# Kernel optimization log

Measured on AMD Instinct MI355X. Metric: run time of the kernel, lower is better.

## Reference

```python
import jax, jax.numpy as jnp
import numpy as np

SEQ, BATCH, IN, H = 1024, 32, 1024, 1024


def setup_inputs() -> dict:
    key = jax.random.key(0)
    ks = jax.random.split(key, 7)
    s_in = 1.0 / np.sqrt(IN)
    s_h = 1.0 / np.sqrt(H)
    return {
        "X": jax.random.normal(ks[0], (SEQ, BATCH, IN), jnp.float32),
        "W_iozfux": jax.random.normal(ks[1], (IN, 5 * H), jnp.float32) * s_in,
        "b_iozfux": jax.random.normal(ks[2], (5 * H,), jnp.float32) * s_in,
        "W_iozfh": jax.random.normal(ks[3], (H, 4 * H), jnp.float32) * s_h,
        "b_iozfh": jax.random.normal(ks[4], (4 * H,), jnp.float32) * s_h,
        "W_um": jax.random.normal(ks[5], (H, H), jnp.float32) * s_h,
        "b_um": jax.random.normal(ks[6], (H,), jnp.float32) * s_h,
    }


def reference(X, W_iozfux, b_iozfux, W_iozfh, b_iozfh, W_um, b_um):
    seq_len, batch, _ = X.shape
    hdim = W_iozfh.shape[0]
    # Input projection has no recurrence: do one big matmul over all timesteps.
    iozfux = jnp.einsum('sbi,ig->sbg', X, W_iozfux) + b_iozfux  # (S, B, 5H)

    h0 = jnp.zeros((batch, hdim), X.dtype)
    c0 = jnp.zeros((batch, hdim), X.dtype)
    ct0 = jnp.tanh(c0)

    def step(carry, ux):
        h, c, c_tanh = carry
        iozf = jax.nn.sigmoid(ux[:, :4 * hdim] + h @ W_iozfh + b_iozfh)
        i, o, z, f = jnp.split(iozf, 4, axis=1)
        u = jnp.tanh(ux[:, 4 * hdim:] + (z * c_tanh) @ W_um + b_um)
        c_new = i * u + f * c
        ct_new = jnp.tanh(c_new)
        h_new = o * ct_new
        return (h_new, c_new, ct_new), h_new

    (h_n, c_n, _), output = jax.lax.scan(step, (h0, c0, ct0), iozfux)
    return output, (h_n[None], c_n[None])
```

## Files before the change

kernel.cpp:

```cpp
#include <hip/hip_runtime.h>


typedef unsigned short u16;
typedef __attribute__((ext_vector_type(4))) float f32x4;
typedef __attribute__((ext_vector_type(8))) short s16x8;
typedef __attribute__((ext_vector_type(8))) unsigned short u16x8;

#define SEQ   1024
#define BATCH 32
#define HDIM  1024
#define GBLK  64

__device__ __forceinline__ u16 f2bf(float f) {
    unsigned u = __builtin_bit_cast(unsigned, f);
    return (u16)((u + 0x7FFFu + ((u >> 16) & 1u)) >> 16);
}
__device__ __forceinline__ float bf2f(u16 h) {
    return __builtin_bit_cast(float, (unsigned)h << 16);
}

__device__ __forceinline__ u16x8 gload_cc(const u16* p) {
    u16x8 v;
    asm volatile("global_load_dwordx4 %0, %1, off sc0 sc1" : "=&v"(v) : "v"(p));
    return v;
}
__device__ __forceinline__ void vmwait0() {
    asm volatile("s_waitcnt vmcnt(0)" ::: "memory");
    __builtin_amdgcn_sched_barrier(0);
}
__device__ __forceinline__ void gstore_cc(u16* p, u16 d) {
    unsigned x = d;
    asm volatile("global_store_short %0, %1, off sc0 sc1" :: "v"(p), "v"(x) : "memory");
}

__global__ void prep_w0(const float* __restrict__ W, const float* __restrict__ b_ux,
                        const float* __restrict__ b_h, const float* __restrict__ b_um,
                        u16* __restrict__ W0p, float* __restrict__ biasp) {
    int p = blockIdx.x;
    int g = p / 80, r = p % 80, gate = r >> 4, j = r & 15;
    int n = 16 * g + j;
    int c = (gate < 4) ? gate * 1024 + n : 4096 + n;
    for (int k = threadIdx.x; k < 1024; k += 256)
        W0p[(long)p * 1024 + k] = f2bf(W[(long)k * 5120 + c]);
    if (threadIdx.x == 0)
        biasp[p] = b_ux[c] + ((gate < 4) ? b_h[gate * 1024 + n] : b_um[n]);
}

__global__ void prep_w1(const float* __restrict__ W, u16* __restrict__ W1p) {
    int qq = blockIdx.x;
    int g = qq >> 6, r = qq & 63, gate = r >> 4, j = r & 15;
    int n = 16 * g + j;
    int c = gate * 1024 + n;
    for (int k = threadIdx.x; k < 1024; k += 256)
        W1p[(long)qq * 1024 + k] = f2bf(W[(long)k * 4096 + c]);
}

__global__ void prep_w2(const float* __restrict__ W, u16* __restrict__ W2p) {
    int n = blockIdx.x;
    for (int k = threadIdx.x; k < 1024; k += 256)
        W2p[(long)n * 1024 + k] = f2bf(W[(long)k * 1024 + n]);
}

__global__ void __launch_bounds__(256) gemm_in(const float* __restrict__ X,
                                               const u16* __restrict__ W0p,
                                               const float* __restrict__ biasp,
                                               u16* __restrict__ Yp) {
    __shared__ u16 As[128 * 40];
    __shared__ u16 Bs[64 * 40];
    const int tid = threadIdx.x, lane = tid & 63, w = tid >> 6;
    const int m = lane & 15, q = lane >> 4;
    const int m0 = blockIdx.y * 128, n0 = blockIdx.x * 64;

    f32x4 acc[2][4];
#pragma unroll
    for (int a = 0; a < 2; ++a)
#pragma unroll
        for (int b = 0; b < 4; ++b) acc[a][b] = (f32x4){0.f, 0.f, 0.f, 0.f};

    const int ar = tid >> 1, as = (tid & 1) * 16;
    const int br = tid >> 2, bs = (tid & 3) * 8;

    for (int k0 = 0; k0 < 1024; k0 += 32) {
        const float* xp = X + (long)(m0 + ar) * 1024 + k0 + as;
        float4 x0 = *(const float4*)(xp);
        float4 x1 = *(const float4*)(xp + 4);
        float4 x2 = *(const float4*)(xp + 8);
        float4 x3 = *(const float4*)(xp + 12);
        u16x8 pa, pb;
        pa[0]=f2bf(x0.x); pa[1]=f2bf(x0.y); pa[2]=f2bf(x0.z); pa[3]=f2bf(x0.w);
        pa[4]=f2bf(x1.x); pa[5]=f2bf(x1.y); pa[6]=f2bf(x1.z); pa[7]=f2bf(x1.w);
        pb[0]=f2bf(x2.x); pb[1]=f2bf(x2.y); pb[2]=f2bf(x2.z); pb[3]=f2bf(x2.w);
        pb[4]=f2bf(x3.x); pb[5]=f2bf(x3.y); pb[6]=f2bf(x3.z); pb[7]=f2bf(x3.w);
        u16x8 bv = *(const u16x8*)(W0p + (long)(n0 + br) * 1024 + k0 + bs);

        *(u16x8*)&As[ar * 40 + as]     = pa;
        *(u16x8*)&As[ar * 40 + as + 8] = pb;
        *(u16x8*)&Bs[br * 40 + bs]     = bv;
        __syncthreads();

        s16x8 a0 = *(const s16x8*)&As[(w * 32 + m) * 40 + q * 8];
        s16x8 a1 = *(const s16x8*)&As[(w * 32 + 16 + m) * 40 + q * 8];
#pragma unroll
        for (int nt = 0; nt < 4; ++nt) {
            s16x8 b = *(const s16x8*)&Bs[(nt * 16 + m) * 40 + q * 8];
            acc[0][nt] = __builtin_amdgcn_mfma_f32_16x16x32_bf16(a0, b, acc[0][nt], 0, 0, 0);
            acc[1][nt] = __builtin_amdgcn_mfma_f32_16x16x32_bf16(a1, b, acc[1][nt], 0, 0, 0);
        }
        __syncthreads();
    }
#pragma unroll
    for (int mt = 0; mt < 2; ++mt)
#pragma unroll
        for (int nt = 0; nt < 4; ++nt) {
            int p = n0 + nt * 16 + m;
            int gg = p / 80, rr = p - gg * 80;
            float bias = biasp[p];
#pragma unroll
            for (int r = 0; r < 4; ++r) {
                int row = m0 + w * 32 + mt * 16 + q * 4 + r;
                int s = row >> 5, b = row & 31;
                Yp[(((long)gg * 1024 + s) * 32 + b) * 80 + rr] = f2bf(acc[mt][nt][r] + bias);
            }
        }
}

__device__ __forceinline__ void gridbar(unsigned* flags, unsigned phase, int g) {
    asm volatile("s_waitcnt vmcnt(0)" ::: "memory");
    __syncthreads();
    if (threadIdx.x < 64) {
        if (threadIdx.x == 0)
            __hip_atomic_store(&flags[g * 32], phase, __ATOMIC_RELEASE,
                               __HIP_MEMORY_SCOPE_AGENT);
        for (;;) {
            unsigned v = __hip_atomic_load(&flags[threadIdx.x * 32], __ATOMIC_RELAXED,
                                           __HIP_MEMORY_SCOPE_AGENT);
            if (__ballot(v >= phase) == ~0ull) break;
            __builtin_amdgcn_s_sleep(1);
        }
    }
    __syncthreads();
}

__global__ void __launch_bounds__(256, 1) ulstm_rec(const u16* __restrict__ W1p,
                                                    const u16* __restrict__ W2p,
                                                    const u16* __restrict__ Yp,
                                                    u16* h_buf, u16* v_buf,
                                                    float* __restrict__ out,
                                                    unsigned* flags) {
    __shared__ u16 stage[32 * 1032];
    __shared__ u16 ys[2][2560];
    __shared__ float gl[4][32][17];
    __shared__ float c_l[32][17], ct_l[32][17];

    const int g = blockIdx.x, tid = threadIdx.x, lane = tid & 63, w = tid >> 6;
    const int m = lane & 15, q = lane >> 4;

    for (int i = tid; i < 512; i += 256) {
        int row = i >> 4, col = i & 15;
        c_l[row][col] = 0.f; ct_l[row][col] = 0.f;
        gstore_cc(&h_buf[row * 1024 + g * 16 + col], (u16)0);
    }
    {
        const u16x8* src = (const u16x8*)(Yp + (long)g * 1024 * 2560);
        for (int i = tid; i < 320; i += 256)
            *(u16x8*)&ys[0][i * 8] = __builtin_nontemporal_load(&src[i]);
    }
    unsigned phase = 1;
    gridbar(flags, phase, g);

    for (int t = 0; t < SEQ; ++t) {
        const u16* ysb = ys[t & 1];

        u16x8 hreg[16];
#pragma unroll
        for (int j = 0; j < 16; ++j) {
            int cch = tid + j * 256;
            int r = cch >> 7, kc = cch & 127;
            hreg[j] = gload_cc(&h_buf[r * 1024 + kc * 8]);
        }
        if (t + 1 < SEQ) {
            const u16x8* src = (const u16x8*)(Yp + ((long)g * 1024 + t + 1) * 2560);
            u16* dst = ys[(t + 1) & 1];
            for (int i = tid; i < 320; i += 256)
                *(u16x8*)&dst[i * 8] = __builtin_nontemporal_load(&src[i]);
        }
        vmwait0();
#pragma unroll
        for (int j = 0; j < 16; ++j) {
            int cch = tid + j * 256;
            int r = cch >> 7, kc = cch & 127;
            *(u16x8*)&stage[r * 1032 + kc * 8] = hreg[j];
        }
        __syncthreads();

        f32x4 acc0 = (f32x4){0.f,0.f,0.f,0.f}, acc1 = (f32x4){0.f,0.f,0.f,0.f};
        {
            const int brow = g * 64 + w * 16 + m;
            const u16* wp = W1p + (long)brow * 1024;
#pragma unroll 8
            for (int kc = 0; kc < 32; ++kc) {
                int k0 = kc * 32 + q * 8;
                s16x8 a0 = *(const s16x8*)&stage[m * 1032 + k0];
                s16x8 a1 = *(const s16x8*)&stage[(16 + m) * 1032 + k0];
                s16x8 b  = *(const s16x8*)&wp[k0];
                acc0 = __builtin_amdgcn_mfma_f32_16x16x32_bf16(a0, b, acc0, 0, 0, 0);
                acc1 = __builtin_amdgcn_mfma_f32_16x16x32_bf16(a1, b, acc1, 0, 0, 0);
            }
        }
#pragma unroll
        for (int r = 0; r < 4; ++r) {
            int row0 = q * 4 + r, row1 = row0 + 16;
            float p0 = acc0[r] + bf2f(ysb[row0 * 80 + w * 16 + m]);
            float p1 = acc1[r] + bf2f(ysb[row1 * 80 + w * 16 + m]);
            float g0 = 1.f / (1.f + __expf(-p0));
            float g1 = 1.f / (1.f + __expf(-p1));
            gl[w][row0][m] = g0;
            gl[w][row1][m] = g1;
            if (w == 2) {
                gstore_cc(&v_buf[row0 * 1024 + g * 16 + m], f2bf(g0 * ct_l[row0][m]));
                gstore_cc(&v_buf[row1 * 1024 + g * 16 + m], f2bf(g1 * ct_l[row1][m]));
            }
        }
        gridbar(flags, ++phase, g);

        u16x8 vreg[16];
#pragma unroll
        for (int j = 0; j < 16; ++j) {
            int cch = tid + j * 256;
            int r = cch >> 7, kc = cch & 127;
            vreg[j] = gload_cc(&v_buf[r * 1024 + kc * 8]);
        }
        vmwait0();
#pragma unroll
        for (int j = 0; j < 16; ++j) {
            int cch = tid + j * 256;
            int r = cch >> 7, kc = cch & 127;
            *(u16x8*)&stage[r * 1032 + kc * 8] = vreg[j];
        }
        __syncthreads();

        if (w < 2) {
            f32x4 acc = (f32x4){0.f,0.f,0.f,0.f};
            const u16* wp = W2p + (long)(g * 16 + m) * 1024;
#pragma unroll 8
            for (int kc = 0; kc < 32; ++kc) {
                int k0 = kc * 32 + q * 8;
                s16x8 a = *(const s16x8*)&stage[(w * 16 + m) * 1032 + k0];
                s16x8 b = *(const s16x8*)&wp[k0];
                acc = __builtin_amdgcn_mfma_f32_16x16x32_bf16(a, b, acc, 0, 0, 0);
            }
#pragma unroll
            for (int r = 0; r < 4; ++r) {
                int row = w * 16 + q * 4 + r;
                float up = acc[r] + bf2f(ysb[row * 80 + 64 + m]);
                float eu = __expf(2.f * up);
                float u = 1.f - 2.f / (eu + 1.f);
                float iv = gl[0][row][m], ov = gl[1][row][m], fv = gl[3][row][m];
                float cv = c_l[row][m];
                float cn = iv * u + fv * cv;
                float ec = __expf(2.f * cn);
                float ctn = 1.f - 2.f / (ec + 1.f);
                float hn = ov * ctn;
                c_l[row][m] = cn;
                ct_l[row][m] = ctn;
                gstore_cc(&h_buf[row * 1024 + g * 16 + m], f2bf(hn));
                __builtin_nontemporal_store(hn, &out[(long)(t * 32 + row) * 1024 + g * 16 + m]);
                if (t == SEQ - 1) {
                    out[33554432l + row * 1024 + g * 16 + m] = hn;
                    out[33554432l + 32768 + row * 1024 + g * 16 + m] = cn;
                }
            }
        }
        gridbar(flags, ++phase, g);
    }
}

extern "C" void kernel_launch(void* const* d_in, const int* in_sizes, int n_in,
                              void* d_out, int out_size, void* d_ws, size_t ws_size,
                              hipStream_t stream) {
    (void)in_sizes; (void)n_in; (void)out_size; (void)ws_size;
    const float* X  = (const float*)d_in[0];
    const float* W0 = (const float*)d_in[1];
    const float* b0 = (const float*)d_in[2];
    const float* W1 = (const float*)d_in[3];
    const float* b1 = (const float*)d_in[4];
    const float* W2 = (const float*)d_in[5];
    const float* b2 = (const float*)d_in[6];
    float* out = (float*)d_out;
    char* ws = (char*)d_ws;

    u16*   Yp    = (u16*)(ws);
    u16*   W0p   = (u16*)(ws + 335544320l);
    u16*   W1p   = (u16*)(ws + 346030080l);
    u16*   W2p   = (u16*)(ws + 354418688l);
    float* biasp = (float*)(ws + 356515840l);
    u16*   h_buf = (u16*)(ws + 356536320l);
    u16*   v_buf = (u16*)(ws + 356601856l);
    unsigned* flags = (unsigned*)(ws + 356667392l);

    hipMemsetAsync(flags, 0, 8192, stream);
    prep_w0<<<5120, 256, 0, stream>>>(W0, b0, b1, b2, W0p, biasp);
    prep_w1<<<4096, 256, 0, stream>>>(W1, W1p);
    prep_w2<<<1024, 256, 0, stream>>>(W2, W2p);
    gemm_in<<<dim3(80, 256), 256, 0, stream>>>(X, W0p, biasp, Yp);

    void* args[] = { (void*)&W1p, (void*)&W2p, (void*)&Yp,
                     (void*)&h_buf, (void*)&v_buf, (void*)&out, (void*)&flags };
    hipLaunchCooperativeKernel(reinterpret_cast<void*>(ulstm_rec),
                               dim3(GBLK), dim3(256), args, 0, stream);
}
```

Before: 14.72 ms.

## Replace grid barriers with flag-tagged data exchange and split-phase barriers

Drops the two full grid barriers per timestep. Each block now publishes its h and v slices as 16-byte packets of seven bf16 values plus a step tag. Consumers poll those packets directly until every tag matches, so the data itself serves as the synchronization signal. Two relaxed counter arrays act as split-phase barriers against buffer reuse, and their waits are overlapped with the gate matmuls. This removes barrier round-trip latency per step, but relies on relaxed ordering and sixteen-bit step tags being correct. It also reuses part of the W0p workspace region for the exchange buffers.

```diff
diff --git a/kernel.cpp b/kernel.cpp
--- a/kernel.cpp
+++ b/kernel.cpp
@@ -19,18 +19,12 @@
     return __builtin_bit_cast(float, (unsigned)h << 16);
 }
 
-__device__ __forceinline__ u16x8 gload_cc(const u16* p) {
-    u16x8 v;
-    asm volatile("global_load_dwordx4 %0, %1, off sc0 sc1" : "=&v"(v) : "v"(p));
-    return v;
-}
 __device__ __forceinline__ void vmwait0() {
     asm volatile("s_waitcnt vmcnt(0)" ::: "memory");
     __builtin_amdgcn_sched_barrier(0);
 }
-__device__ __forceinline__ void gstore_cc(u16* p, u16 d) {
-    unsigned x = d;
-    asm volatile("global_store_short %0, %1, off sc0 sc1" :: "v"(p), "v"(x) : "memory");
+__device__ __forceinline__ void gstore_cc16(u16* p, u16x8 d) {
+    asm volatile("global_store_dwordx4 %0, %1, off sc0 sc1" :: "v"(p), "v"(d) : "memory");
 }
 
 __global__ void prep_w0(const float* __restrict__ W, const float* __restrict__ b_ux,
@@ -124,33 +118,51 @@
         }
 }
 
-__device__ __forceinline__ void gridbar(unsigned* flags, unsigned phase, int g) {
-    asm volatile("s_waitcnt vmcnt(0)" ::: "memory");
-    __syncthreads();
-    if (threadIdx.x < 64) {
-        if (threadIdx.x == 0)
-            __hip_atomic_store(&flags[g * 32], phase, __ATOMIC_RELEASE,
-                               __HIP_MEMORY_SCOPE_AGENT);
-        for (;;) {
-            unsigned v = __hip_atomic_load(&flags[threadIdx.x * 32], __ATOMIC_RELAXED,
-                                           __HIP_MEMORY_SCOPE_AGENT);
-            if (__ballot(v >= phase) == ~0ull) break;
-            __builtin_amdgcn_s_sleep(1);
-        }
-    }
-    __syncthreads();
+#define ISSUE1(i, ofs)                                                        \
+    if (!((valid >> i) & 1))                                                  \
+        asm volatile("global_load_dwordx4 %0, %1, off offset:" ofs " sc0 sc1" \
+                     : "=&v"(ch[i]) : "v"(lanebase));
+
+__device__ __forceinline__ void poll_unpack(const u16* lanebase, unsigned valid,
+                                            u16 want, u16* stage_, int tid) {
+    u16x8 ch[24];
+    int rounds = 0;
+    while (valid != 0xFFFFFFu) {
+        if (rounds++) __builtin_amdgcn_s_sleep(1);
+        ISSUE1(0, "0")   ISSUE1(1, "16")   ISSUE1(2, "32")   ISSUE1(3, "48")
+        ISSUE1(4, "64")  ISSUE1(5, "80")   ISSUE1(6, "96")   ISSUE1(7, "112")
+        ISSUE1(8, "128") ISSUE1(9, "144")  ISSUE1(10, "160") ISSUE1(11, "176")
+        ISSUE1(12, "192") ISSUE1(13, "208") ISSUE1(14, "224") ISSUE1(15, "240")
+        ISSUE1(16, "256") ISSUE1(17, "272") ISSUE1(18, "288") ISSUE1(19, "304")
+        ISSUE1(20, "320") ISSUE1(21, "336") ISSUE1(22, "352") ISSUE1(23, "368")
+        vmwait0();
+#pragma unroll
+        for (int i = 0; i < 24; ++i) {
+            if (!((valid >> i) & 1) && ch[i][7] == want) {
+                valid |= 1u << i;
+                const int grp = tid * 8 + i / 3;
+                const int row = grp >> 6, gg = grp & 63;
+                const int col0 = gg * 16 + (i % 3) * 7;
+                const int n = (i % 3 == 2) ? 2 : 7;
+#pragma unroll
+                for (int j = 0; j < 7; ++j)
+                    if (j < n) stage_[row * 1032 + col0 + j] = ch[i][j];
+            }
+        }
+    }
 }
 
 __global__ void __launch_bounds__(256, 1) ulstm_rec(const u16* __restrict__ W1p,
                                                     const u16* __restrict__ W2p,
                                                     const u16* __restrict__ Yp,
-                                                    u16* h_buf, u16* v_buf,
+                                                    u16* hx, u16* vx,
                                                     float* __restrict__ out,
-                                                    unsigned* flags) {
+                                                    unsigned* bar1, unsigned* bar2) {
     __shared__ u16 stage[32 * 1032];
     __shared__ u16 ys[2][2560];
     __shared__ float gl[4][32][17];
     __shared__ float c_l[32][17], ct_l[32][17];
+    __shared__ u16 h_l[32 * 17 + 8];
 
     const int g = blockIdx.x, tid = threadIdx.x, lane = tid & 63, w = tid >> 6;
     const int m = lane & 15, q = lane >> 4;
@@ -158,40 +170,53 @@
     for (int i = tid; i < 512; i += 256) {
         int row = i >> 4, col = i & 15;
         c_l[row][col] = 0.f; ct_l[row][col] = 0.f;
-        gstore_cc(&h_buf[row * 1024 + g * 16 + col], (u16)0);
+    }
+    for (int i = tid; i < 32 * 17 + 8; i += 256) h_l[i] = 0;
+
+    if (tid < 96) {
+        int row = (tid * 171) >> 9, c = tid - 3 * row;
+        u16x8 z = (u16x8){0, 0, 0, 0, 0, 0, 0, 0};
+        z[7] = (u16)1;
+        gstore_cc16(hx + (row * 64 + g) * 24 + c * 8, z);
     }
     {
         const u16x8* src = (const u16x8*)(Yp + (long)g * 1024 * 2560);
         for (int i = tid; i < 320; i += 256)
             *(u16x8*)&ys[0][i * 8] = __builtin_nontemporal_load(&src[i]);
     }
-    unsigned phase = 1;
-    gridbar(flags, phase, g);
+
+    unsigned selfmask = 0;
+#pragma unroll
+    for (int i = 0; i < 24; ++i)
+        if (((tid * 8 + i / 3) & 63) == g) selfmask |= 1u << i;
+    const int prow = tid >> 3, pcp = (tid & 7) * 2;
+
+    __syncthreads();
 
     for (int t = 0; t < SEQ; ++t) {
         const u16* ysb = ys[t & 1];
-
-        u16x8 hreg[16];
-#pragma unroll
-        for (int j = 0; j < 16; ++j) {
-            int cch = tid + j * 256;
-            int r = cch >> 7, kc = cch & 127;
-            hreg[j] = gload_cc(&h_buf[r * 1024 + kc * 8]);
-        }
+        const u16 want = (u16)(t + 1);
+
         if (t + 1 < SEQ) {
             const u16x8* src = (const u16x8*)(Yp + ((long)g * 1024 + t + 1) * 2560);
             u16* dst = ys[(t + 1) & 1];
             for (int i = tid; i < 320; i += 256)
                 *(u16x8*)&dst[i * 8] = __builtin_nontemporal_load(&src[i]);
         }
-        vmwait0();
-#pragma unroll
-        for (int j = 0; j < 16; ++j) {
-            int cch = tid + j * 256;
-            int r = cch >> 7, kc = cch & 127;
-            *(u16x8*)&stage[r * 1032 + kc * 8] = hreg[j];
-        }
-        __syncthreads();
+
+        stage[prow * 1032 + g * 16 + pcp]     = h_l[prow * 17 + pcp];
+        stage[prow * 1032 + g * 16 + pcp + 1] = h_l[prow * 17 + pcp + 1];
+        poll_unpack(hx + (t & 1) * 49152 + tid * 192, selfmask, want, stage, tid);
+        __syncthreads();
+
+        unsigned fl = 0;
+        if (w == 0) {
+            if (tid == 0)
+                __hip_atomic_store(&bar1[g * 32], (unsigned)(t + 1),
+                                   __ATOMIC_RELAXED, __HIP_MEMORY_SCOPE_AGENT);
+            fl = __hip_atomic_load(&bar2[lane * 32], __ATOMIC_RELAXED,
+                                   __HIP_MEMORY_SCOPE_AGENT);
+        }
 
         f32x4 acc0 = (f32x4){0.f,0.f,0.f,0.f}, acc1 = (f32x4){0.f,0.f,0.f,0.f};
         {
@@ -214,30 +239,44 @@
             float p1 = acc1[r] + bf2f(ysb[row1 * 80 + w * 16 + m]);
             float g0 = 1.f / (1.f + __expf(-p0));
             float g1 = 1.f / (1.f + __expf(-p1));
-            gl[w][row0][m] = g0;
-            gl[w][row1][m] = g1;
             if (w == 2) {
-                gstore_cc(&v_buf[row0 * 1024 + g * 16 + m], f2bf(g0 * ct_l[row0][m]));
-                gstore_cc(&v_buf[row1 * 1024 + g * 16 + m], f2bf(g1 * ct_l[row1][m]));
-            }
-        }
-        gridbar(flags, ++phase, g);
-
-        u16x8 vreg[16];
-#pragma unroll
-        for (int j = 0; j < 16; ++j) {
-            int cch = tid + j * 256;
-            int r = cch >> 7, kc = cch & 127;
-            vreg[j] = gload_cc(&v_buf[r * 1024 + kc * 8]);
-        }
-        vmwait0();
-#pragma unroll
-        for (int j = 0; j < 16; ++j) {
-            int cch = tid + j * 256;
-            int r = cch >> 7, kc = cch & 127;
-            *(u16x8*)&stage[r * 1032 + kc * 8] = vreg[j];
-        }
-        __syncthreads();
+                gl[2][row0][m] = g0 * ct_l[row0][m];
+                gl[2][row1][m] = g1 * ct_l[row1][m];
+            } else {
+                gl[w][row0][m] = g0;
+                gl[w][row1][m] = g1;
+            }
+        }
+        if (w == 0 && t >= 1) {
+            while (__ballot((int)fl >= t - 1) != ~0ull) {
+                __builtin_amdgcn_s_sleep(1);
+                fl = __hip_atomic_load(&bar2[lane * 32], __ATOMIC_RELAXED,
+                                       __HIP_MEMORY_SCOPE_AGENT);
+            }
+        }
+        __syncthreads();
+
+        if (tid < 96) {
+            int row = (tid * 171) >> 9, c = tid - 3 * row;
+            u16x8 pk;
+#pragma unroll
+            for (int j = 0; j < 7; ++j) pk[j] = f2bf(gl[2][row][c * 7 + j]);
+            pk[7] = want;
+            gstore_cc16(vx + (t & 1) * 49152 + (row * 64 + g) * 24 + c * 8, pk);
+        }
+
+        stage[prow * 1032 + g * 16 + pcp]     = f2bf(gl[2][prow][pcp]);
+        stage[prow * 1032 + g * 16 + pcp + 1] = f2bf(gl[2][prow][pcp + 1]);
+        poll_unpack(vx + (t & 1) * 49152 + tid * 192, selfmask, want, stage, tid);
+        __syncthreads();
+
+        if (tid == 0)
+            __hip_atomic_store(&bar2[g * 32], (unsigned)(t + 1),
+                               __ATOMIC_RELAXED, __HIP_MEMORY_SCOPE_AGENT);
+        unsigned fl2 = 0;
+        if (w == 3)
+            fl2 = __hip_atomic_load(&bar1[lane * 32], __ATOMIC_RELAXED,
+                                    __HIP_MEMORY_SCOPE_AGENT);
 
         if (w < 2) {
             f32x4 acc = (f32x4){0.f,0.f,0.f,0.f};
@@ -263,7 +302,7 @@
                 float hn = ov * ctn;
                 c_l[row][m] = cn;
                 ct_l[row][m] = ctn;
-                gstore_cc(&h_buf[row * 1024 + g * 16 + m], f2bf(hn));
+                h_l[row * 17 + m] = f2bf(hn);
                 __builtin_nontemporal_store(hn, &out[(long)(t * 32 + row) * 1024 + g * 16 + m]);
                 if (t == SEQ - 1) {
                     out[33554432l + row * 1024 + g * 16 + m] = hn;
@@ -271,7 +310,23 @@
                 }
             }
         }
-        gridbar(flags, ++phase, g);
+        if (w == 3) {
+            while (__ballot((int)fl2 >= t) != ~0ull) {
+                __builtin_amdgcn_s_sleep(1);
+                fl2 = __hip_atomic_load(&bar1[lane * 32], __ATOMIC_RELAXED,
+                                        __HIP_MEMORY_SCOPE_AGENT);
+            }
+        }
+        __syncthreads();
+
+        if (t + 1 < SEQ && tid < 96) {
+            int row = (tid * 171) >> 9, c = tid - 3 * row;
+            u16x8 pk;
+#pragma unroll
+            for (int j = 0; j < 7; ++j) pk[j] = h_l[row * 17 + c * 7 + j];
+            pk[7] = (u16)(t + 2);
+            gstore_cc16(hx + ((t + 1) & 1) * 49152 + (row * 64 + g) * 24 + c * 8, pk);
+        }
     }
 }
 
@@ -294,18 +349,21 @@
     u16*   W1p   = (u16*)(ws + 346030080l);
     u16*   W2p   = (u16*)(ws + 354418688l);
     float* biasp = (float*)(ws + 356515840l);
-    u16*   h_buf = (u16*)(ws + 356536320l);
-    u16*   v_buf = (u16*)(ws + 356601856l);
-    unsigned* flags = (unsigned*)(ws + 356667392l);
-
-    hipMemsetAsync(flags, 0, 8192, stream);
+
+    u16*   hx    = (u16*)(ws + 335544320l);
+    u16*   vx    = (u16*)(ws + 335740928l);
+    unsigned* bar1 = (unsigned*)(ws + 335937536l);
+    unsigned* bar2 = (unsigned*)(ws + 335945728l);
+
     prep_w0<<<5120, 256, 0, stream>>>(W0, b0, b1, b2, W0p, biasp);
     prep_w1<<<4096, 256, 0, stream>>>(W1, W1p);
     prep_w2<<<1024, 256, 0, stream>>>(W2, W2p);
     gemm_in<<<dim3(80, 256), 256, 0, stream>>>(X, W0p, biasp, Yp);
+    hipMemsetAsync(hx, 0, 409600, stream);
 
     void* args[] = { (void*)&W1p, (void*)&W2p, (void*)&Yp,
-                     (void*)&h_buf, (void*)&v_buf, (void*)&out, (void*)&flags };
+                     (void*)&hx, (void*)&vx, (void*)&out,
+                     (void*)&bar1, (void*)&bar2 };
     hipLaunchCooperativeKernel(reinterpret_cast<void*>(ulstm_rec),
                                dim3(GBLK), dim3(256), args, 0, stream);
 }
```

Measured after the change: 23.01 ms. 1.56x slower.

## Consolidate recurrent LSTM into 16 workgroups of 1024 threads

Applied to the files above, without the earlier changes.

The persistent recurrent kernel now runs on 16 cooperative blocks of 1024 threads instead of 64 blocks of 256. Each block owns 64 hidden columns, so one fewer tier of blocks takes part in each grid barrier. Each block also stages h/v once per step for four times the work, which cuts redundant global reads of the shared state. The Y prefetch is held in registers and written to LDS after the barrier, and the barrier polls only active flags. The trade-off is fewer CUs doing the per-step matmul and larger per-block LDS and register pressure.

```diff
diff --git a/kernel.cpp b/kernel.cpp
--- a/kernel.cpp
+++ b/kernel.cpp
@@ -9,7 +9,7 @@
 #define SEQ   1024
 #define BATCH 32
 #define HDIM  1024
-#define GBLK  64
+#define GBLK  16
 
 __device__ __forceinline__ u16 f2bf(float f) {
     unsigned u = __builtin_bit_cast(unsigned, f);
@@ -128,12 +128,15 @@
     asm volatile("s_waitcnt vmcnt(0)" ::: "memory");
     __syncthreads();
     if (threadIdx.x < 64) {
+        unsigned v;
         if (threadIdx.x == 0)
             __hip_atomic_store(&flags[g * 32], phase, __ATOMIC_RELEASE,
                                __HIP_MEMORY_SCOPE_AGENT);
         for (;;) {
-            unsigned v = __hip_atomic_load(&flags[threadIdx.x * 32], __ATOMIC_RELAXED,
-                                           __HIP_MEMORY_SCOPE_AGENT);
+            v = (threadIdx.x < GBLK)
+                    ? __hip_atomic_load(&flags[threadIdx.x * 32], __ATOMIC_RELAXED,
+                                        __HIP_MEMORY_SCOPE_AGENT)
+                    : phase;
             if (__ballot(v >= phase) == ~0ull) break;
             __builtin_amdgcn_s_sleep(1);
         }
@@ -141,133 +144,159 @@
     __syncthreads();
 }
 
-__global__ void __launch_bounds__(256, 1) ulstm_rec(const u16* __restrict__ W1p,
-                                                    const u16* __restrict__ W2p,
-                                                    const u16* __restrict__ Yp,
-                                                    u16* h_buf, u16* v_buf,
-                                                    float* __restrict__ out,
-                                                    unsigned* flags) {
-    __shared__ u16 stage[32 * 1032];
-    __shared__ u16 ys[2][2560];
-    __shared__ float gl[4][32][17];
-    __shared__ float c_l[32][17], ct_l[32][17];
+__global__ void __launch_bounds__(1024, 1) ulstm_rec(const u16* __restrict__ W1p,
+                                                     const u16* __restrict__ W2p,
+                                                     const u16* __restrict__ Yp,
+                                                     u16* h_buf, u16* v_buf,
+                                                     float* __restrict__ out,
+                                                     unsigned* flags) {
+    __shared__ u16 stage[32 * 1028];
+    __shared__ u16 ys[2][4][2560];
+    __shared__ float gl[4][32][66];
+    __shared__ float c_l[32][66], ct_l[32][66];
 
     const int g = blockIdx.x, tid = threadIdx.x, lane = tid & 63, w = tid >> 6;
     const int m = lane & 15, q = lane >> 4;
-
-    for (int i = tid; i < 512; i += 256) {
-        int row = i >> 4, col = i & 15;
-        c_l[row][col] = 0.f; ct_l[row][col] = 0.f;
-        gstore_cc(&h_buf[row * 1024 + g * 16 + col], (u16)0);
+    const int nb = g * 64;
+
+    for (int i = tid; i < 32 * 66; i += 1024) {
+        ((float*)c_l)[i] = 0.f; ((float*)ct_l)[i] = 0.f;
+    }
+    for (int i = tid; i < 2048; i += 1024) {
+        int row = i >> 6, col = i & 63;
+        gstore_cc(&h_buf[row * 1024 + nb + col], (u16)0);
     }
     {
-        const u16x8* src = (const u16x8*)(Yp + (long)g * 1024 * 2560);
-        for (int i = tid; i < 320; i += 256)
-            *(u16x8*)&ys[0][i * 8] = __builtin_nontemporal_load(&src[i]);
+        for (int i = tid; i < 1280; i += 1024) {
+            int cb = i / 320, wi = i - cb * 320;
+            const u16x8* src = (const u16x8*)(Yp + (long)(4 * g + cb) * 1024 * 2560);
+            *(u16x8*)&ys[0][cb][wi * 8] = __builtin_nontemporal_load(&src[wi]);
+        }
     }
     unsigned phase = 1;
     gridbar(flags, phase, g);
 
     for (int t = 0; t < SEQ; ++t) {
-        const u16* ysb = ys[t & 1];
-
-        u16x8 hreg[16];
-#pragma unroll
-        for (int j = 0; j < 16; ++j) {
-            int cch = tid + j * 256;
-            int r = cch >> 7, kc = cch & 127;
-            hreg[j] = gload_cc(&h_buf[r * 1024 + kc * 8]);
-        }
+        const u16 (*ysb)[2560] = ys[t & 1];
+
+        u16x8 yreg[2];
+        int yi0 = tid, yi1 = tid + 1024;
         if (t + 1 < SEQ) {
-            const u16x8* src = (const u16x8*)(Yp + ((long)g * 1024 + t + 1) * 2560);
-            u16* dst = ys[(t + 1) & 1];
-            for (int i = tid; i < 320; i += 256)
-                *(u16x8*)&dst[i * 8] = __builtin_nontemporal_load(&src[i]);
+            {
+                int cb = yi0 / 320, wi = yi0 - cb * 320;
+                const u16x8* src = (const u16x8*)(Yp + ((long)(4 * g + cb) * 1024 + t + 1) * 2560);
+                yreg[0] = __builtin_nontemporal_load(&src[wi]);
+            }
+            if (yi1 < 1280) {
+                int cb = yi1 / 320, wi = yi1 - cb * 320;
+                const u16x8* src = (const u16x8*)(Yp + ((long)(4 * g + cb) * 1024 + t + 1) * 2560);
+                yreg[1] = __builtin_nontemporal_load(&src[wi]);
+            }
+        }
+        u16x8 hreg[4];
+#pragma unroll
+        for (int j = 0; j < 4; ++j) {
+            int idx = tid + j * 1024;
+            hreg[j] = gload_cc(&h_buf[(idx >> 7) * 1024 + (idx & 127) * 8]);
         }
         vmwait0();
 #pragma unroll
-        for (int j = 0; j < 16; ++j) {
-            int cch = tid + j * 256;
-            int r = cch >> 7, kc = cch & 127;
-            *(u16x8*)&stage[r * 1032 + kc * 8] = hreg[j];
+        for (int j = 0; j < 4; ++j) {
+            int idx = tid + j * 1024;
+            *(u16x8*)&stage[(idx >> 7) * 1028 + (idx & 127) * 8] = hreg[j];
         }
         __syncthreads();
 
+        const int gw = w >> 2, cb = w & 3;
         f32x4 acc0 = (f32x4){0.f,0.f,0.f,0.f}, acc1 = (f32x4){0.f,0.f,0.f,0.f};
         {
-            const int brow = g * 64 + w * 16 + m;
+            const int brow = (4 * g + cb) * 64 + gw * 16 + m;
             const u16* wp = W1p + (long)brow * 1024;
 #pragma unroll 8
             for (int kc = 0; kc < 32; ++kc) {
                 int k0 = kc * 32 + q * 8;
-                s16x8 a0 = *(const s16x8*)&stage[m * 1032 + k0];
-                s16x8 a1 = *(const s16x8*)&stage[(16 + m) * 1032 + k0];
+                s16x8 a0 = *(const s16x8*)&stage[m * 1028 + k0];
+                s16x8 a1 = *(const s16x8*)&stage[(16 + m) * 1028 + k0];
                 s16x8 b  = *(const s16x8*)&wp[k0];
                 acc0 = __builtin_amdgcn_mfma_f32_16x16x32_bf16(a0, b, acc0, 0, 0, 0);
                 acc1 = __builtin_amdgcn_mfma_f32_16x16x32_bf16(a1, b, acc1, 0, 0, 0);
             }
         }
-#pragma unroll
-        for (int r = 0; r < 4; ++r) {
-            int row0 = q * 4 + r, row1 = row0 + 16;
-            float p0 = acc0[r] + bf2f(ysb[row0 * 80 + w * 16 + m]);
-            float p1 = acc1[r] + bf2f(ysb[row1 * 80 + w * 16 + m]);
-            float g0 = 1.f / (1.f + __expf(-p0));
-            float g1 = 1.f / (1.f + __expf(-p1));
-            gl[w][row0][m] = g0;
-            gl[w][row1][m] = g1;
-            if (w == 2) {
-                gstore_cc(&v_buf[row0 * 1024 + g * 16 + m], f2bf(g0 * ct_l[row0][m]));
-                gstore_cc(&v_buf[row1 * 1024 + g * 16 + m], f2bf(g1 * ct_l[row1][m]));
+        {
+            const int col = cb * 16 + m;
+#pragma unroll
+            for (int r = 0; r < 4; ++r) {
+                int row0 = q * 4 + r, row1 = row0 + 16;
+                float p0 = acc0[r] + bf2f(ysb[cb][row0 * 80 + gw * 16 + m]);
+                float p1 = acc1[r] + bf2f(ysb[cb][row1 * 80 + gw * 16 + m]);
+                float g0 = 1.f / (1.f + __expf(-p0));
+                float g1 = 1.f / (1.f + __expf(-p1));
+                if (gw == 2) {
+                    gstore_cc(&v_buf[row0 * 1024 + nb + col], f2bf(g0 * ct_l[row0][col]));
+                    gstore_cc(&v_buf[row1 * 1024 + nb + col], f2bf(g1 * ct_l[row1][col]));
+                } else {
+                    gl[gw][row0][col] = g0;
+                    gl[gw][row1][col] = g1;
+                }
             }
         }
         gridbar(flags, ++phase, g);
 
-        u16x8 vreg[16];
-#pragma unroll
-        for (int j = 0; j < 16; ++j) {
-            int cch = tid + j * 256;
-            int r = cch >> 7, kc = cch & 127;
-            vreg[j] = gload_cc(&v_buf[r * 1024 + kc * 8]);
+        if (t + 1 < SEQ) {
+            {
+                int cb2 = yi0 / 320, wi = yi0 - cb2 * 320;
+                *(u16x8*)&ys[(t + 1) & 1][cb2][wi * 8] = yreg[0];
+            }
+            if (yi1 < 1280) {
+                int cb2 = yi1 / 320, wi = yi1 - cb2 * 320;
+                *(u16x8*)&ys[(t + 1) & 1][cb2][wi * 8] = yreg[1];
+            }
+        }
+        u16x8 vreg[4];
+#pragma unroll
+        for (int j = 0; j < 4; ++j) {
+            int idx = tid + j * 1024;
+            vreg[j] = gload_cc(&v_buf[(idx >> 7) * 1024 + (idx & 127) * 8]);
         }
         vmwait0();
 #pragma unroll
-        for (int j = 0; j < 16; ++j) {
-            int cch = tid + j * 256;
-            int r = cch >> 7, kc = cch & 127;
-            *(u16x8*)&stage[r * 1032 + kc * 8] = vreg[j];
+        for (int j = 0; j < 4; ++j) {
+            int idx = tid + j * 1024;
+            *(u16x8*)&stage[(idx >> 7) * 1028 + (idx & 127) * 8] = vreg[j];
         }
         __syncthreads();
 
-        if (w < 2) {
+        if (w < 8) {
+            const int rh = w & 1, cb2 = w >> 1;
+            const int col = cb2 * 16 + m;
             f32x4 acc = (f32x4){0.f,0.f,0.f,0.f};
-            const u16* wp = W2p + (long)(g * 16 + m) * 1024;
+            const u16* wp = W2p + (long)(nb + col) * 1024;
 #pragma unroll 8
             for (int kc = 0; kc < 32; ++kc) {
                 int k0 = kc * 32 + q * 8;
-                s16x8 a = *(const s16x8*)&stage[(w * 16 + m) * 1032 + k0];
+                s16x8 a = *(const s16x8*)&stage[(rh * 16 + m) * 1028 + k0];
                 s16x8 b = *(const s16x8*)&wp[k0];
                 acc = __builtin_amdgcn_mfma_f32_16x16x32_bf16(a, b, acc, 0, 0, 0);
             }
 #pragma unroll
             for (int r = 0; r < 4; ++r) {
-                int row = w * 16 + q * 4 + r;
-                float up = acc[r] + bf2f(ysb[row * 80 + 64 + m]);
+                int row = rh * 16 + q * 4 + r;
+                float up = acc[r] + bf2f(ysb[cb2][row * 80 + 64 + m]);
                 float eu = __expf(2.f * up);
                 float u = 1.f - 2.f / (eu + 1.f);
-                float iv = gl[0][row][m], ov = gl[1][row][m], fv = gl[3][row][m];
-                float cv = c_l[row][m];
+                float iv = gl[0][row][col], ov = gl[1][row][col], fv = gl[3][row][col];
+                float cv = c_l[row][col];
                 float cn = iv * u + fv * cv;
                 float ec = __expf(2.f * cn);
                 float ctn = 1.f - 2.f / (ec + 1.f);
                 float hn = ov * ctn;
-                c_l[row][m] = cn;
-                ct_l[row][m] = ctn;
-                gstore_cc(&h_buf[row * 1024 + g * 16 + m], f2bf(hn));
-                __builtin_nontemporal_store(hn, &out[(long)(t * 32 + row) * 1024 + g * 16 + m]);
+                c_l[row][col] = cn;
+                ct_l[row][col] = ctn;
+                gstore_cc(&h_buf[row * 1024 + nb + col], f2bf(hn));
+                __builtin_nontemporal_store(hn, &out[(long)(t * 32 + row) * 1024 + nb + col]);
                 if (t == SEQ - 1) {
-                    out[33554432l + row * 1024 + g * 16 + m] = hn;
-                    out[33554432l + 32768 + row * 1024 + g * 16 + m] = cn;
+                    out[33554432l + row * 1024 + nb + col] = hn;
+                    out[33554432l + 32768 + row * 1024 + nb + col] = cn;
                 }
             }
         }
@@ -307,5 +336,5 @@
     void* args[] = { (void*)&W1p, (void*)&W2p, (void*)&Yp,
                      (void*)&h_buf, (void*)&v_buf, (void*)&out, (void*)&flags };
     hipLaunchCooperativeKernel(reinterpret_cast<void*>(ulstm_rec),
-                               dim3(GBLK), dim3(256), args, 0, stream);
-}
+                               dim3(GBLK), dim3(1024), args, 0, stream);
+}
```

New measurement: 30.13 ms. 105% more time.
